# Optimization experiments

Measured on AMD Instinct MI355X. Metric: run time of the kernel, lower is better.

## Reference

```python
import jax, jax.numpy as jnp
import numpy as np

B, S, ENC, DEC, ATT = 32, 2048, 1024, 1024, 1024


def setup_inputs() -> dict:
    key = jax.random.key(0)
    k1, k2, k3, k4, k5, k6 = jax.random.split(key, 6)
    sc = lambda fan_in: 1.0 / np.sqrt(fan_in)
    return {
        "encoder_hidden_states": jax.random.normal(k1, (B, S, ENC), dtype=jnp.float32),
        "decoder_hidden_state": jax.random.normal(k2, (B, 1, DEC), dtype=jnp.float32),
        # nn.Linear stores weight as [out, in]; we keep [in, out] for x @ W
        "U_a": jax.random.uniform(k3, (ENC, ATT), jnp.float32, -sc(ENC), sc(ENC)),
        "W_a": jax.random.uniform(k4, (DEC, ATT), jnp.float32, -sc(DEC), sc(DEC)),
        "v_t": jax.random.uniform(k5, (ATT, 1), jnp.float32, -sc(ATT), sc(ATT)),
        "ffn": jax.random.uniform(k6, (ENC + DEC, DEC), jnp.float32, -sc(ENC + DEC), sc(ENC + DEC)),
    }


def reference(encoder_hidden_states, decoder_hidden_state, U_a, W_a, v_t, ffn):
    # additive (Bahdanau) attention
    u = jnp.einsum('bse,ea->bsa', encoder_hidden_states, U_a)      # [B,S,A]
    w = jnp.einsum('bqd,da->bqa', decoder_hidden_state, W_a)       # [B,1,A]
    e = jnp.tanh(w + u) @ v_t                                      # [B,S,1]
    align = jax.nn.softmax(e, axis=1)                              # softmax over seq
    # context = alignment^T @ encoder_states  -> [B,1,E]
    context = jnp.einsum('bsq,bse->bqe', align, encoder_hidden_states)
    cat = jnp.concatenate([decoder_hidden_state, context], axis=-1)  # [B,1,D+E]
    output = jnp.tanh(cat @ ffn)                                     # [B,1,D]
    return (output, context)
```

## Files before the change

### kernel.cpp

```cpp
#include <hip/hip_runtime.h>
#include <hip/hip_bf16.h>
#include <cstdint>
#include <cstddef>

#define B_  32
#define S_  2048
#define E_  1024
#define A_  1024
#define D_  1024
#define M_TOT (B_ * S_)

typedef __attribute__((ext_vector_type(8))) __bf16 bf16x8;
typedef __attribute__((ext_vector_type(4))) float  f32x4;

__device__ __forceinline__ float fast_tanh(float x) {
    float cx = fminf(fmaxf(x, -15.f), 15.f);
    float e2 = __expf(2.f * cx);
    return 1.f - 2.f / (e2 + 1.f);
}

__device__ __forceinline__ bf16x8 pack8(float4 f0, float4 f1) {
    bf16x8 r;
    r[0] = (__bf16)f0.x; r[1] = (__bf16)f0.y; r[2] = (__bf16)f0.z; r[3] = (__bf16)f0.w;
    r[4] = (__bf16)f1.x; r[5] = (__bf16)f1.y; r[6] = (__bf16)f1.z; r[7] = (__bf16)f1.w;
    return r;
}

typedef __attribute__((address_space(3))) uint32_t lds_u32_t;
typedef __attribute__((address_space(1))) const uint32_t gbl_u32_t;
__device__ __forceinline__ void async_ld16(const void* g, void* l) {
    __builtin_amdgcn_global_load_lds((gbl_u32_t*)g,
                                     (lds_u32_t*)(uint32_t)(uintptr_t)l,
                                     16, 0, 0);
}

__global__ __launch_bounds__(256) void k_cvt(const float* __restrict__ enc,
                                             __bf16* __restrict__ encB) {
    size_t base = (size_t)blockIdx.x * 8192 + (size_t)threadIdx.x * 8;
    #pragma unroll
    for (int it = 0; it < 4; ++it) {
        size_t idx = base + (size_t)it * 2048;
        float4 f0 = *(const float4*)(enc + idx);
        float4 f1 = *(const float4*)(enc + idx + 4);
        *(bf16x8*)(encB + idx) = pack8(f0, f1);
    }
}

__global__ __launch_bounds__(256) void k_trans_U(const float* __restrict__ Ua,
                                                 __bf16* __restrict__ Ut) {
    __shared__ float tile[64][65];
    int bid = blockIdx.x;
    int k0 = (bid >> 4) * 64, n0 = (bid & 15) * 64;
    int t = threadIdx.x;
    int r = t >> 6, c = t & 63;
    #pragma unroll
    for (int i = 0; i < 16; ++i)
        tile[i * 4 + r][c] = Ua[(size_t)(k0 + i * 4 + r) * 1024 + n0 + c];
    __syncthreads();
    #pragma unroll
    for (int i = 0; i < 16; ++i)
        Ut[(size_t)(n0 + i * 4 + r) * 1024 + k0 + c] = (__bf16)tile[c][i * 4 + r];
}

__global__ __launch_bounds__(256) void k_w_part(const float* __restrict__ dec,
                                                const float* __restrict__ Wa,
                                                float* __restrict__ w_part) {
    int bid = blockIdx.x;
    int ac = bid & 3, b = (bid >> 2) & 31, kc = bid >> 7;
    int a = ac * 256 + threadIdx.x;
    int k0 = kc * 128;
    float acc = 0.f;
    #pragma unroll 8
    for (int k = 0; k < 128; ++k)
        acc += dec[b * 1024 + k0 + k] * Wa[(size_t)(k0 + k) * 1024 + a];
    w_part[kc * 32768 + b * 1024 + a] = acc;
}

#define PBAR  __builtin_amdgcn_s_barrier()
#define LGKM0 asm volatile("s_waitcnt lgkmcnt(0)" ::: "memory")

#define DS_A(mh) do { \
    _Pragma("unroll") for (int mf = 0; mf < 4; ++mf) \
        _Pragma("unroll") for (int k2 = 0; k2 < 2; ++k2) \
            a[mf][k2] = *(const bf16x8*)&L[buf][0][(wm + (mh)*64 + mf*16 + c)*64 + (((k2*4 + q) ^ (c & 7)))*8]; \
} while (0)

#define DS_B(nh, bb) do { \
    _Pragma("unroll") for (int nf = 0; nf < 2; ++nf) \
        _Pragma("unroll") for (int k2 = 0; k2 < 2; ++k2) \
            bb[nf][k2] = *(const bf16x8*)&L[buf][1][(wn + (nh)*32 + nf*16 + c)*64 + (((k2*4 + q) ^ (c & 7)))*8]; \
} while (0)

#define MMA_Q(mh, nh, bb) do { \
    __builtin_amdgcn_s_setprio(1); \
    _Pragma("unroll") for (int mf = 0; mf < 4; ++mf) \
        _Pragma("unroll") for (int nf = 0; nf < 2; ++nf) \
            _Pragma("unroll") for (int k2 = 0; k2 < 2; ++k2) \
                acc[(mh)*4 + mf][(nh)*2 + nf] = __builtin_amdgcn_mfma_f32_16x16x32_bf16( \
                    a[mf][k2], bb[nf][k2], acc[(mh)*4 + mf][(nh)*2 + nf], 0, 0, 0); \
    __builtin_amdgcn_s_setprio(0); \
} while (0)

__global__ __launch_bounds__(512, 2) void k_gemm8(
        const __bf16* __restrict__ encB, const __bf16* __restrict__ Ut,
        const float* __restrict__ w_part, const float* __restrict__ v,
        float* __restrict__ e_part) {
    __shared__ __bf16 L[2][2][16384];

    const int t = threadIdx.x;
    const int wid = t >> 6, lane = t & 63;
    const int q = lane >> 4, c = lane & 15;
    const int wm = (wid >> 2) * 128;
    const int wn = (wid & 3) * 64;

    const int p = blockIdx.x;
    const int xcd = p & 7, j = p >> 3;
    const int m_tile = xcd * 32 + (j >> 2);
    const int n_tile = j & 3;
    const int m0 = m_tile * 256, n0 = n_tile * 256;

    const int scol = ((lane & 7) ^ (lane >> 3)) * 8;
    const __bf16* gA = encB + (size_t)(m0 + (t >> 3)) * 1024 + scol;
    const __bf16* gB = Ut   + (size_t)(n0 + (t >> 3)) * 1024 + scol;
    const int ldsoff0 = wid * 512;

    auto stage = [&](int kind, int h, int kt2) {
        const __bf16* src = (kind ? gB : gA) + (size_t)h * 128 * 1024 + (size_t)kt2 * 64;
        __bf16* dst = &L[kt2 & 1][kind][h * 8192 + ldsoff0];
        async_ld16(src,             dst);
        async_ld16(src + 64 * 1024, dst + 4096);
    };

    f32x4 acc[8][4];
    #pragma unroll
    for (int i = 0; i < 8; ++i)
        #pragma unroll
        for (int jj = 0; jj < 4; ++jj)
            #pragma unroll
            for (int r = 0; r < 4; ++r) acc[i][jj][r] = 0.f;

    bf16x8 a[4][2], b0[2][2], b1[2][2];

    stage(0, 0, 0); stage(1, 0, 0); stage(0, 1, 0); stage(1, 1, 0);
    stage(0, 0, 1); stage(1, 0, 1);
    asm volatile("s_waitcnt vmcnt(4)" ::: "memory");
    PBAR;
    __builtin_amdgcn_sched_barrier(0);

    #pragma unroll 2
    for (int kt = 0; kt < 16; ++kt) {
        const int buf = kt & 1;
        DS_A(0);
        DS_B(0, b0);
        if (kt < 15) { stage(0, 1, kt + 1); stage(1, 1, kt + 1); }
        PBAR; LGKM0;
        MMA_Q(0, 0, b0);
        PBAR;
        DS_B(1, b1);
        PBAR; LGKM0;
        MMA_Q(0, 1, b1);
        PBAR;
        DS_A(1);
        PBAR; LGKM0;
        MMA_Q(1, 1, b1);
        PBAR;
        if (kt < 14) { stage(0, 0, kt + 2); stage(1, 0, kt + 2); }
        PBAR;
        MMA_Q(1, 0, b0);
        if (kt < 15) {
            if (kt < 14) asm volatile("s_waitcnt vmcnt(4)" ::: "memory");
            else         asm volatile("s_waitcnt vmcnt(0)" ::: "memory");
            PBAR;
            __builtin_amdgcn_sched_barrier(0);
        }
    }

    __syncthreads();
    float* e_red = (float*)&L[0][0][0];

    const int b_idx = m0 >> 11;
    float wv[4], vv[4];
    #pragma unroll
    for (int nf = 0; nf < 4; ++nf) {
        int col = n0 + wn + nf * 16 + c;
        float s = 0.f;
        #pragma unroll
        for (int pp = 0; pp < 8; ++pp) s += w_part[pp * 32768 + b_idx * 1024 + col];
        wv[nf] = s;
        vv[nf] = v[col];
    }
    #pragma unroll
    for (int mf = 0; mf < 8; ++mf) {
        float s0 = 0.f, s1 = 0.f, s2 = 0.f, s3 = 0.f;
        #pragma unroll
        for (int nf = 0; nf < 4; ++nf) {
            s0 += fast_tanh(wv[nf] + acc[mf][nf][0]) * vv[nf];
            s1 += fast_tanh(wv[nf] + acc[mf][nf][1]) * vv[nf];
            s2 += fast_tanh(wv[nf] + acc[mf][nf][2]) * vv[nf];
            s3 += fast_tanh(wv[nf] + acc[mf][nf][3]) * vv[nf];
        }
        #pragma unroll
        for (int off = 1; off < 16; off <<= 1) {
            s0 += __shfl_xor(s0, off, 16);
            s1 += __shfl_xor(s1, off, 16);
            s2 += __shfl_xor(s2, off, 16);
            s3 += __shfl_xor(s3, off, 16);
        }
        if (c == 0) {
            int row = wm + mf * 16 + q * 4;
            e_red[(wid & 3) * 256 + row + 0] = s0;
            e_red[(wid & 3) * 256 + row + 1] = s1;
            e_red[(wid & 3) * 256 + row + 2] = s2;
            e_red[(wid & 3) * 256 + row + 3] = s3;
        }
    }
    __syncthreads();
    if (t < 256)
        e_part[(size_t)n_tile * M_TOT + m0 + t] =
            e_red[t] + e_red[256 + t] + e_red[512 + t] + e_red[768 + t];
}

__global__ __launch_bounds__(256) void k_gemm_fb(
        const float* __restrict__ enc, const __bf16* __restrict__ Ut,
        const float* __restrict__ w_part, const float* __restrict__ v,
        float* __restrict__ e_part) {
    __shared__ __bf16 lX[2][128 * 32];
    __shared__ __bf16 lU[2][128 * 32];
    __shared__ float  e_lds[2][128];

    const int t = threadIdx.x;
    const int bid = blockIdx.x;
    const int xcd = bid & 7;
    const int j_  = bid >> 3;
    const int m_tile = xcd * 64 + (j_ >> 3);
    const int n_tile = j_ & 7;
    const int m0 = m_tile * 128;
    const int n0 = n_tile * 128;
    const int wave = t >> 6;
    const int lane = t & 63;
    const int q = lane >> 4;
    const int c = lane & 15;
    const int wm = (wave >> 1) * 64;
    const int wn = (wave & 1) * 64;

    f32x4 acc[4][4];
    #pragma unroll
    for (int i = 0; i < 4; ++i)
        #pragma unroll
        for (int j = 0; j < 4; ++j)
            #pragma unroll
            for (int r = 0; r < 4; ++r) acc[i][j][r] = 0.f;

    const int lrow = lane >> 2;
    const int p    = lane & 3;
    const int sw   = (lrow >> 1) & 3;
    const int lcolS = ((p ^ sw)) * 8;
    const int xrow = wave * 32;

    const float*  gxa = enc + (size_t)(m0 + xrow + lrow) * 1024 + lcolS;
    const __bf16* gub = Ut  + (size_t)(n0 + xrow + lrow) * 1024 + lcolS;

    float4 f0, f1, f2, f3;
    auto loadA = [&](int kk) {
        const float* pp = gxa + kk;
        f0 = *(const float4*)pp;
        f1 = *(const float4*)(pp + 4);
        f2 = *(const float4*)(pp + 16 * 1024);
        f3 = *(const float4*)(pp + 16 * 1024 + 4);
    };
    auto writeA = [&](int bsel) {
        *(bf16x8*)(&lX[bsel][(xrow + lrow) * 32 + p * 8])      = pack8(f0, f1);
        *(bf16x8*)(&lX[bsel][(xrow + 16 + lrow) * 32 + p * 8]) = pack8(f2, f3);
    };
    auto stageB = [&](int kk, int bsel) {
        async_ld16(gub + kk,             &lU[bsel][xrow * 32]);
        async_ld16(gub + kk + 16 * 1024, &lU[bsel][(xrow + 16) * 32]);
    };
    const int fcol = (q ^ ((c >> 1) & 3)) * 8;
    auto compute = [&](int bsel) {
        bf16x8 af[4], bfr[4];
        #pragma unroll
        for (int i = 0; i < 4; ++i)
            af[i] = *(const bf16x8*)(&lX[bsel][(wm + i * 16 + c) * 32 + fcol]);
        #pragma unroll
        for (int j = 0; j < 4; ++j)
            bfr[j] = *(const bf16x8*)(&lU[bsel][(wn + j * 16 + c) * 32 + fcol]);
        #pragma unroll
        for (int i = 0; i < 4; ++i)
            #pragma unroll
            for (int j = 0; j < 4; ++j)
                acc[i][j] = __builtin_amdgcn_mfma_f32_16x16x32_bf16(af[i], bfr[j], acc[i][j], 0, 0, 0);
    };

    loadA(0);
    stageB(0, 0);
    writeA(0);
    __syncthreads();
    for (int kk = 0; kk < 1024; kk += 64) {
        if (kk + 32 < 1024) { loadA(kk + 32); stageB(kk + 32, 1); }
        compute(0);
        if (kk + 32 < 1024) writeA(1);
        __syncthreads();
        if (kk + 64 < 1024) { loadA(kk + 64); stageB(kk + 64, 0); }
        compute(1);
        if (kk + 64 < 1024) writeA(0);
        __syncthreads();
    }

    const int b_idx = m0 >> 11;
    float wv[4], vv[4];
    #pragma unroll
    for (int j = 0; j < 4; ++j) {
        int col = n0 + wn + j * 16 + c;
        float s = 0.f;
        #pragma unroll
        for (int pp = 0; pp < 8; ++pp) s += w_part[pp * 32768 + b_idx * 1024 + col];
        wv[j] = s;
        vv[j] = v[col];
    }
    #pragma unroll
    for (int i = 0; i < 4; ++i) {
        float s0 = 0.f, s1 = 0.f, s2 = 0.f, s3 = 0.f;
        #pragma unroll
        for (int j = 0; j < 4; ++j) {
            s0 += fast_tanh(wv[j] + acc[i][j][0]) * vv[j];
            s1 += fast_tanh(wv[j] + acc[i][j][1]) * vv[j];
            s2 += fast_tanh(wv[j] + acc[i][j][2]) * vv[j];
            s3 += fast_tanh(wv[j] + acc[i][j][3]) * vv[j];
        }
        #pragma unroll
        for (int off = 1; off < 16; off <<= 1) {
            s0 += __shfl_xor(s0, off, 16);
            s1 += __shfl_xor(s1, off, 16);
            s2 += __shfl_xor(s2, off, 16);
            s3 += __shfl_xor(s3, off, 16);
        }
        if (c == 0) {
            int row = wm + i * 16 + q * 4;
            e_lds[wave & 1][row + 0] = s0;
            e_lds[wave & 1][row + 1] = s1;
            e_lds[wave & 1][row + 2] = s2;
            e_lds[wave & 1][row + 3] = s3;
        }
    }
    __syncthreads();
    if (t < 128)
        e_part[(size_t)n_tile * M_TOT + m0 + t] = e_lds[0][t] + e_lds[1][t];
}

template<int NP>
__global__ __launch_bounds__(256) void k_softmax(const float* __restrict__ ep,
                                                 float* __restrict__ al) {
    int b = blockIdx.x, t = threadIdx.x;
    float ev[8];
    #pragma unroll
    for (int i = 0; i < 8; ++i) {
        int s = i * 256 + t;
        float x = 0.f;
        #pragma unroll
        for (int p = 0; p < NP; ++p) x += ep[p * M_TOT + b * 2048 + s];
        ev[i] = x;
    }
    float mx = ev[0];
    #pragma unroll
    for (int i = 1; i < 8; ++i) mx = fmaxf(mx, ev[i]);
    #pragma unroll
    for (int off = 1; off < 64; off <<= 1) mx = fmaxf(mx, __shfl_xor(mx, off, 64));
    __shared__ float redm[4];
    if ((t & 63) == 0) redm[t >> 6] = mx;
    __syncthreads();
    mx = fmaxf(fmaxf(redm[0], redm[1]), fmaxf(redm[2], redm[3]));

    float ex[8], sm = 0.f;
    #pragma unroll
    for (int i = 0; i < 8; ++i) { ex[i] = __expf(ev[i] - mx); sm += ex[i]; }
    #pragma unroll
    for (int off = 1; off < 64; off <<= 1) sm += __shfl_xor(sm, off, 64);
    __shared__ float reds[4];
    if ((t & 63) == 0) reds[t >> 6] = sm;
    __syncthreads();
    sm = reds[0] + reds[1] + reds[2] + reds[3];
    float inv = 1.f / sm;
    #pragma unroll
    for (int i = 0; i < 8; ++i) al[b * 2048 + i * 256 + t] = ex[i] * inv;
}

__global__ __launch_bounds__(256) void k_ctx(const float* __restrict__ enc,
                                             const float* __restrict__ al,
                                             float* __restrict__ ctx_part) {
    int b  = blockIdx.x >> 5;
    int sc = blockIdx.x & 31;
    int t  = threadIdx.x;
    int e4 = t * 4;
    float ax = 0.f, ay = 0.f, az = 0.f, aw = 0.f;
    int sbase = sc * 64;
    for (int i = 0; i < 64; i += 4) {
        #pragma unroll
        for (int u = 0; u < 4; ++u) {
            int s = sbase + i + u;
            float a = al[b * 2048 + s];
            float4 x = *(const float4*)(enc + (size_t)(b * 2048 + s) * 1024 + e4);
            ax += a * x.x; ay += a * x.y; az += a * x.z; aw += a * x.w;
        }
    }
    float4 r; r.x = ax; r.y = ay; r.z = az; r.w = aw;
    *(float4*)(ctx_part + ((size_t)sc * 32 + b) * 1024 + e4) = r;
}

__global__ __launch_bounds__(256) void k_final(const float* __restrict__ dec,
                                               const float* __restrict__ ffn,
                                               const float* __restrict__ ctx_part,
                                               float* __restrict__ out) {
    int b  = blockIdx.x >> 4;
    int dc = blockIdx.x & 15;
    int t  = threadIdx.x;
    __shared__ float cat[2048];
    __shared__ float red[4][64];

    #pragma unroll
    for (int r = 0; r < 4; ++r) {
        int e = r * 256 + t;
        cat[e] = dec[b * 1024 + e];
        float s = 0.f;
        #pragma unroll
        for (int p = 0; p < 32; ++p) s += ctx_part[((size_t)p * 32 + b) * 1024 + e];
        cat[1024 + e] = s;
        if (dc == 0) out[32768 + b * 1024 + e] = s;
    }
    __syncthreads();

    int dl = t & 63, ic = t >> 6;
    int d  = dc * 64 + dl;
    float acc = 0.f;
    int i0 = ic * 512;
    for (int i = 0; i < 512; i += 4) {
        float4 cv = *(const float4*)(cat + i0 + i);
        const float* fr = ffn + (size_t)(i0 + i) * 1024 + d;
        acc += cv.x * fr[0];
        acc += cv.y * fr[1024];
        acc += cv.z * fr[2048];
        acc += cv.w * fr[3072];
    }
    red[ic][dl] = acc;
    __syncthreads();
    if (t < 64) {
        float s = red[0][t] + red[1][t] + red[2][t] + red[3][t];
        out[b * 1024 + dc * 64 + t] = fast_tanh(s);
    }
}

extern "C" void kernel_launch(void* const* d_in, const int* in_sizes, int n_in,
                              void* d_out, int out_size, void* d_ws, size_t ws_size,
                              hipStream_t stream) {
    const float* enc = (const float*)d_in[0];
    const float* dec = (const float*)d_in[1];
    const float* Ua  = (const float*)d_in[2];
    const float* Wa  = (const float*)d_in[3];
    const float* vt  = (const float*)d_in[4];
    const float* ffn = (const float*)d_in[5];
    float* out = (float*)d_out;

    char* ws = (char*)d_ws;
    size_t off = 0;
    __bf16* Ut       = (__bf16*)(ws + off); off += (size_t)A_ * E_ * 2;
    float*  e_part   = (float*)(ws + off);  off += (size_t)8 * M_TOT * 4;
    float*  al       = (float*)(ws + off);  off += (size_t)M_TOT * 4;
    float*  w_part   = (float*)(ws + off);  off += (size_t)8 * B_ * 1024 * 4;
    float*  ctx_part = (float*)(ws + off);  off += (size_t)32 * B_ * 1024 * 4;
    __bf16* encB     = (__bf16*)(ws + off); off += (size_t)M_TOT * E_ * 2;
    const bool use_async = ws_size >= off;

    k_trans_U<<<256, 256, 0, stream>>>(Ua, Ut);
    k_w_part<<<1024, 256, 0, stream>>>(dec, Wa, w_part);
    if (use_async) {
        k_cvt<<<8192, 256, 0, stream>>>(enc, encB);
        k_gemm8<<<1024, 512, 0, stream>>>(encB, Ut, w_part, vt, e_part);
        k_softmax<4><<<B_, 256, 0, stream>>>(e_part, al);
    } else {
        k_gemm_fb<<<4096, 256, 0, stream>>>(enc, Ut, w_part, vt, e_part);
        k_softmax<8><<<B_, 256, 0, stream>>>(e_part, al);
    }
    k_ctx<<<B_ * 32, 256, 0, stream>>>(enc, al, ctx_part);
    k_final<<<B_ * 16, 256, 0, stream>>>(dec, ffn, ctx_part, out);
}
```

Measured before the change: 631.8 us.

## Merge prep kernels into one launch and restructure GEMM k-loop pipelining

Folds the bf16 conversion, U transpose and W partial GEMV into one multi-role prep kernel, which removes two launches and lets the small jobs run alongside the conversion. The main GEMM's per-wave row mapping is interleaved (64-row halves spaced 128 apart). Its k-loop now issues most of the next tile's loads early, cuts the number of barriers and explicit lgkmcnt waits, and loads both B fragments before the MMAs. The fallback path now writes encB through the prep kernel, which may overrun a workspace that is too small for it, and the tighter schedule relies on the compiler inserting correct LDS waits.

```diff
diff --git a/kernel.cpp b/kernel.cpp
--- a/kernel.cpp
+++ b/kernel.cpp
@@ -34,55 +34,56 @@
                                      16, 0, 0);
 }
 
-__global__ __launch_bounds__(256) void k_cvt(const float* __restrict__ enc,
-                                             __bf16* __restrict__ encB) {
-    size_t base = (size_t)blockIdx.x * 8192 + (size_t)threadIdx.x * 8;
-    #pragma unroll
-    for (int it = 0; it < 4; ++it) {
-        size_t idx = base + (size_t)it * 2048;
-        float4 f0 = *(const float4*)(enc + idx);
-        float4 f1 = *(const float4*)(enc + idx + 4);
-        *(bf16x8*)(encB + idx) = pack8(f0, f1);
-    }
-}
-
-__global__ __launch_bounds__(256) void k_trans_U(const float* __restrict__ Ua,
-                                                 __bf16* __restrict__ Ut) {
+__global__ __launch_bounds__(256) void k_prep(const float* __restrict__ enc,
+                                              __bf16* __restrict__ encB,
+                                              const float* __restrict__ Ua,
+                                              __bf16* __restrict__ Ut,
+                                              const float* __restrict__ dec,
+                                              const float* __restrict__ Wa,
+                                              float* __restrict__ w_part) {
     __shared__ float tile[64][65];
     int bid = blockIdx.x;
-    int k0 = (bid >> 4) * 64, n0 = (bid & 15) * 64;
     int t = threadIdx.x;
-    int r = t >> 6, c = t & 63;
-    #pragma unroll
-    for (int i = 0; i < 16; ++i)
-        tile[i * 4 + r][c] = Ua[(size_t)(k0 + i * 4 + r) * 1024 + n0 + c];
-    __syncthreads();
-    #pragma unroll
-    for (int i = 0; i < 16; ++i)
-        Ut[(size_t)(n0 + i * 4 + r) * 1024 + k0 + c] = (__bf16)tile[c][i * 4 + r];
-}
-
-__global__ __launch_bounds__(256) void k_w_part(const float* __restrict__ dec,
-                                                const float* __restrict__ Wa,
-                                                float* __restrict__ w_part) {
-    int bid = blockIdx.x;
-    int ac = bid & 3, b = (bid >> 2) & 31, kc = bid >> 7;
-    int a = ac * 256 + threadIdx.x;
-    int k0 = kc * 128;
-    float acc = 0.f;
-    #pragma unroll 8
-    for (int k = 0; k < 128; ++k)
-        acc += dec[b * 1024 + k0 + k] * Wa[(size_t)(k0 + k) * 1024 + a];
-    w_part[kc * 32768 + b * 1024 + a] = acc;
+    if (bid < 8192) {
+        size_t base = (size_t)bid * 8192 + (size_t)t * 8;
+        #pragma unroll
+        for (int it = 0; it < 4; ++it) {
+            size_t idx = base + (size_t)it * 2048;
+            float4 f0 = *(const float4*)(enc + idx);
+            float4 f1 = *(const float4*)(enc + idx + 4);
+            *(bf16x8*)(encB + idx) = pack8(f0, f1);
+        }
+    } else if (bid < 8448) {
+        int b2 = bid - 8192;
+        int k0 = (b2 >> 4) * 64, n0 = (b2 & 15) * 64;
+        int r = t >> 6, c = t & 63;
+        #pragma unroll
+        for (int i = 0; i < 16; ++i)
+            tile[i * 4 + r][c] = Ua[(size_t)(k0 + i * 4 + r) * 1024 + n0 + c];
+        __syncthreads();
+        #pragma unroll
+        for (int i = 0; i < 16; ++i)
+            Ut[(size_t)(n0 + i * 4 + r) * 1024 + k0 + c] = (__bf16)tile[c][i * 4 + r];
+    } else {
+        int b3 = bid - 8448;
+        int ac = b3 & 3, b = (b3 >> 2) & 31, kc = b3 >> 7;
+        int a = ac * 256 + t;
+        int k0 = kc * 128;
+        float acc = 0.f;
+        #pragma unroll 8
+        for (int k = 0; k < 128; ++k)
+            acc += dec[b * 1024 + k0 + k] * Wa[(size_t)(k0 + k) * 1024 + a];
+        w_part[kc * 32768 + b * 1024 + a] = acc;
+    }
 }
 
 #define PBAR  __builtin_amdgcn_s_barrier()
-#define LGKM0 asm volatile("s_waitcnt lgkmcnt(0)" ::: "memory")
+#define SCHED0 __builtin_amdgcn_sched_barrier(0)
 
 #define DS_A(mh) do { \
     _Pragma("unroll") for (int mf = 0; mf < 4; ++mf) \
         _Pragma("unroll") for (int k2 = 0; k2 < 2; ++k2) \
-            a[mf][k2] = *(const bf16x8*)&L[buf][0][(wm + (mh)*64 + mf*16 + c)*64 + (((k2*4 + q) ^ (c & 7)))*8]; \
+            a[mf][k2] = *(const bf16x8*)&L[buf][0][(wmb + (mh)*128 + mf*16 + c)*64 + (((k2*4 + q) ^ (c & 7)))*8]; \
 } while (0)
 
 #define DS_B(nh, bb) do { \
@@ -110,8 +111,8 @@
     const int t = threadIdx.x;
     const int wid = t >> 6, lane = t & 63;
     const int q = lane >> 4, c = lane & 15;
-    const int wm = (wid >> 2) * 128;
-    const int wn = (wid & 3) * 64;
+    const int wmb = (wid >> 2) * 64;
+    const int wn  = (wid & 3) * 64;
 
     const int p = blockIdx.x;
     const int xcd = p & 7, j = p >> 3;
@@ -141,37 +142,30 @@
 
     bf16x8 a[4][2], b0[2][2], b1[2][2];
 
-    stage(0, 0, 0); stage(1, 0, 0); stage(0, 1, 0); stage(1, 1, 0);
-    stage(0, 0, 1); stage(1, 0, 1);
-    asm volatile("s_waitcnt vmcnt(4)" ::: "memory");
-    PBAR;
-    __builtin_amdgcn_sched_barrier(0);
+    stage(0, 0, 0); stage(1, 0, 0); stage(1, 1, 0);
+    stage(0, 1, 0);
+    asm volatile("s_waitcnt vmcnt(2)" ::: "memory");
+    PBAR; SCHED0;
 
     #pragma unroll 2
     for (int kt = 0; kt < 16; ++kt) {
         const int buf = kt & 1;
         DS_A(0);
         DS_B(0, b0);
-        if (kt < 15) { stage(0, 1, kt + 1); stage(1, 1, kt + 1); }
-        PBAR; LGKM0;
+        DS_B(1, b1);
+        if (kt < 15) { stage(0, 0, kt + 1); stage(1, 0, kt + 1); stage(1, 1, kt + 1); }
         MMA_Q(0, 0, b0);
-        PBAR;
-        DS_B(1, b1);
-        PBAR; LGKM0;
         MMA_Q(0, 1, b1);
-        PBAR;
+        if (kt < 15) asm volatile("s_waitcnt vmcnt(6)" ::: "memory");
+        else         asm volatile("s_waitcnt vmcnt(0)" ::: "memory");
+        PBAR; SCHED0;
         DS_A(1);
-        PBAR; LGKM0;
+        if (kt < 15) stage(0, 1, kt + 1);
+        MMA_Q(1, 0, b0);
         MMA_Q(1, 1, b1);
-        PBAR;
-        if (kt < 14) { stage(0, 0, kt + 2); stage(1, 0, kt + 2); }
-        PBAR;
-        MMA_Q(1, 0, b0);
         if (kt < 15) {
-            if (kt < 14) asm volatile("s_waitcnt vmcnt(4)" ::: "memory");
-            else         asm volatile("s_waitcnt vmcnt(0)" ::: "memory");
-            PBAR;
-            __builtin_amdgcn_sched_barrier(0);
+            asm volatile("s_waitcnt vmcnt(2)" ::: "memory");
+            PBAR; SCHED0;
         }
     }
 
@@ -190,14 +184,14 @@
         vv[nf] = v[col];
     }
     #pragma unroll
-    for (int mf = 0; mf < 8; ++mf) {
+    for (int mf8 = 0; mf8 < 8; ++mf8) {
         float s0 = 0.f, s1 = 0.f, s2 = 0.f, s3 = 0.f;
         #pragma unroll
         for (int nf = 0; nf < 4; ++nf) {
-            s0 += fast_tanh(wv[nf] + acc[mf][nf][0]) * vv[nf];
-            s1 += fast_tanh(wv[nf] + acc[mf][nf][1]) * vv[nf];
-            s2 += fast_tanh(wv[nf] + acc[mf][nf][2]) * vv[nf];
-            s3 += fast_tanh(wv[nf] + acc[mf][nf][3]) * vv[nf];
+            s0 += fast_tanh(wv[nf] + acc[mf8][nf][0]) * vv[nf];
+            s1 += fast_tanh(wv[nf] + acc[mf8][nf][1]) * vv[nf];
+            s2 += fast_tanh(wv[nf] + acc[mf8][nf][2]) * vv[nf];
+            s3 += fast_tanh(wv[nf] + acc[mf8][nf][3]) * vv[nf];
         }
         #pragma unroll
         for (int off = 1; off < 16; off <<= 1) {
@@ -207,7 +201,8 @@
             s3 += __shfl_xor(s3, off, 16);
         }
         if (c == 0) {
-            int row = wm + mf * 16 + q * 4;
+            int mh = mf8 >> 2, mfl = mf8 & 3;
+            int row = wmb + mh * 128 + mfl * 16 + q * 4;
             e_red[(wid & 3) * 256 + row + 0] = s0;
             e_red[(wid & 3) * 256 + row + 1] = s1;
             e_red[(wid & 3) * 256 + row + 2] = s2;
@@ -470,13 +465,12 @@
     __bf16* encB     = (__bf16*)(ws + off); off += (size_t)M_TOT * E_ * 2;
     const bool use_async = ws_size >= off;
 
-    k_trans_U<<<256, 256, 0, stream>>>(Ua, Ut);
-    k_w_part<<<1024, 256, 0, stream>>>(dec, Wa, w_part);
     if (use_async) {
-        k_cvt<<<8192, 256, 0, stream>>>(enc, encB);
+        k_prep<<<9472, 256, 0, stream>>>(enc, encB, Ua, Ut, dec, Wa, w_part);
         k_gemm8<<<1024, 512, 0, stream>>>(encB, Ut, w_part, vt, e_part);
         k_softmax<4><<<B_, 256, 0, stream>>>(e_part, al);
     } else {
+        k_prep<<<9472, 256, 0, stream>>>(enc, encB, Ua, Ut, dec, Wa, w_part);
         k_gemm_fb<<<4096, 256, 0, stream>>>(enc, Ut, w_part, vt, e_part);
         k_softmax<8><<<B_, 256, 0, stream>>>(e_part, al);
     }
```

New measurement: 613.1 us. 1.03x faster.
